# Optimization experiments

Hardware: AMD Instinct MI355X
Metric: run time of the kernel (lower is better)

## Reference

```python
import jax, jax.numpy as jnp
import numpy as np

SCALES = (3, 9, 17, 33)  # must be odd so padding=s//2 preserves spatial size


def _box_conv(img, s):
    # img: [B,1,H,W]; conv with an all-ones s x s kernel, 'same' padding for odd s
    k = jnp.ones((1, 1, s, s), img.dtype)
    p = s // 2
    return jax.lax.conv_general_dilated(
        img, k, window_strides=(1, 1), padding=[(p, p), (p, p)],
        dimension_numbers=("NCHW", "OIHW", "NCHW"))


def setup_inputs() -> dict:
    key = jax.random.key(0)
    B, C, H, W = 8, 3, 1024, 1024
    x = jax.random.normal(key, (B, C, H, W), dtype=jnp.float32)
    # mimicking sparse path-traced samples
    keep = jax.random.uniform(jax.random.fold_in(key, 1), (B, 1, H, W)) >= 0.3
    x = jnp.where(keep, x, 0.0)
    return {"x": x}


def reference(x):
    # F.conv2d(x, ones(1,3,1,1)/3) == per-pixel mean over the 3 channels
    lum = jnp.mean(x, axis=1, keepdims=True)          # [B,1,H,W]
    nonzero = (lum != 0).astype(lum.dtype)            # [B,1,H,W]
    feats = []
    for s in SCALES:
        count = _box_conv(nonzero, s)                 # number of nonzero pixels in window
        pool = _box_conv(lum, s) / jnp.maximum(count, 1.0)  # mean over nonzero pixels
        feats.append(count / float(s * s))            # percentage of nonzero pixels
        feats.append(pool)
    return jnp.concatenate(feats, axis=1)             # [B, 2*len(SCALES), H, W]
```

## Files before the change

kernel.cpp:

```cpp
#include <hip/hip_runtime.h>


constexpr int THREADS = 256;
constexpr int LOADW   = 256;
constexpr int HALO    = 17;
constexpr int COUT    = 223;
constexpr int RING2   = 19;
constexpr int ROWSEG  = 32;

constexpr int    Wc  = 1024;
constexpr int    Hc  = 1024;
constexpr size_t HWc = (size_t)Hc * Wc;

__device__ __forceinline__ void barrier_lds() {
    asm volatile("s_waitcnt lgkmcnt(0)" ::: "memory");
    __builtin_amdgcn_s_barrier();
    __builtin_amdgcn_sched_barrier(0);
}

template<int CTRL, int RM>
__device__ __forceinline__ int dppadd_i(int v) {
    int sh = __builtin_amdgcn_update_dpp(0, v, CTRL, RM, 0xF, true);
    return v + sh;
}

__device__ __forceinline__ int wave_iscan_i(int v) {
    v = dppadd_i<0x111, 0xF>(v);
    v = dppadd_i<0x112, 0xF>(v);
    v = dppadd_i<0x114, 0xF>(v);
    v = dppadd_i<0x118, 0xF>(v);
    v = dppadd_i<0x142, 0xA>(v);
    v = dppadd_i<0x143, 0xC>(v);
    return v;
}

__device__ __forceinline__ int sx16(unsigned v) {
    return (int)(short)(unsigned short)v;
}

__global__ __launch_bounds__(THREADS, 5)
void nzfeat_kernel(const float* __restrict__ x, float* __restrict__ out) {
    constexpr int   PP[4]   = {1, 4, 8, 16};
    constexpr float INVA[4] = {1.f/9.f, 1.f/81.f, 1.f/289.f, 1.f/1089.f};
    constexpr float INVQ    = 1.f / 1024.f;

    __shared__ unsigned int   ringL[RING2][LOADW];
    __shared__ unsigned short ringN[RING2][LOADW];
    __shared__ int2           wsum[2][2][4];

    const int t    = threadIdx.x;
    const int lane = t & 63;
    const int wv   = t >> 6;

    const int x0 = blockIdx.x * COUT;
    const int y0 = blockIdx.y * ROWSEG;
    const int b  = blockIdx.z;

    const int    gx   = x0 - HALO + t;
    const bool   gxok = (gx >= 0) && (gx < Wc);
    const int    gxc  = min(max(gx, 0), Wc - 1);
    const float* xb   = x + (size_t)b * 3 * HWc + gxc;

    auto load_row = [&](int r, float& a0, float& a1, float& a2) {
        const int rc = min(max(r, 0), Hc - 1);
        const float* p = xb + ((size_t)rc << 10);
        a0 = p[0]; a1 = p[HWc]; a2 = p[2 * HWc];
    };

    auto ps2  = [&](int j) { return (int)((unsigned)(j + 190) % (unsigned)RING2); };
    auto wpos = [&](int v) { return v >= RING2 ? v - RING2 : v; };
    auto wneg = [&](int v) { return v < 0 ? v + RING2 : v; };

    auto scan_local = [&](float c0, float c1, float c2, int r, int par, int which) -> int2 {
        float lum = 0.f;
        if (gxok && (unsigned)r < (unsigned)Hc)
            lum = (c0 + c1 + c2) * (1.0f / 3.0f);
        const bool nzb = (lum != 0.f);
        unsigned long long m = __ballot(nzb);
        int below = __builtin_amdgcn_mbcnt_hi((unsigned)(m >> 32),
                      __builtin_amdgcn_mbcnt_lo((unsigned)m, 0));
        int np = below + (nzb ? 1 : 0);
        int q  = (int)rintf(lum * 1024.f);
        int lp = wave_iscan_i(q);
        if (lane == 63) wsum[par][which][wv] = make_int2(lp, np);
        return make_int2(lp, np);
    };

    auto combine_write = [&](int par, int2 A, int2 Bv, int pslot) {
        int oAl = 0, oAn = 0, oBl = 0, oBn = 0;
        #pragma unroll
        for (int w2 = 0; w2 < 3; ++w2)
            if (w2 < wv) {
                int2 u = wsum[par][0][w2]; int2 v = wsum[par][1][w2];
                oAl += u.x; oAn += u.y; oBl += v.x; oBn += v.y;
            }
        unsigned llo = (unsigned)(A.x + oAl) & 0xFFFFu;
        unsigned lhi = (unsigned)(Bv.x + oBl) & 0xFFFFu;
        ringL[pslot][t] = (lhi << 16) | llo;
        unsigned nlo = (unsigned)(A.y + oAn) & 0xFFu;
        unsigned nhi = (unsigned)(Bv.y + oBn) & 0xFFu;
        ringN[pslot][t] = (unsigned short)((nhi << 8) | nlo);
    };

    auto rdAligned = [&](int s, int x1, int d, int& dl0, int& dl1,
                         int& dn0, int& dn1) {
        const unsigned int* Lp = &ringL[s][x1];
        unsigned w0 = Lp[0], w1 = Lp[d];
        dl0 = sx16(w1 - w0);
        dl1 = sx16((w1 >> 16) - (w0 >> 16));
        const unsigned short* Np = &ringN[s][x1];
        unsigned n0 = Np[0], n1 = Np[d];
        dn0 = (int)((n1 - n0) & 0xFFu);
        dn1 = (int)(((n1 >> 8) - (n0 >> 8)) & 0xFFu);
    };
    auto rdStraddle = [&](int sH, int sL2, int x1, int d, int& dA, int& dB,
                          int& nA, int& nB) {
        const unsigned int* LpH = &ringL[sH][x1];
        unsigned h0 = LpH[0], h1 = LpH[d];
        dA = sx16((h1 >> 16) - (h0 >> 16));
        const unsigned int* LpL = &ringL[sL2][x1];
        unsigned l0 = LpL[0], l1 = LpL[d];
        dB = sx16(l1 - l0);
        const unsigned short* NpH = &ringN[sH][x1];
        unsigned m0 = NpH[0], m1 = NpH[d];
        nA = (int)(((m1 >> 8) - (m0 >> 8)) & 0xFFu);
        const unsigned short* NpL = &ringN[sL2][x1];
        unsigned k0 = NpL[0], k1 = NpL[d];
        nB = (int)((k1 - k0) & 0xFFu);
    };

    float a0, a1, a2, b0c, b1c, b2c;
    load_row(y0 - 18, a0, a1, a2);
    load_row(y0 - 17, b0c, b1c, b2c);
    for (int i = 0; i < 17; ++i) {
        const int rA = y0 - 18 + 2 * i;
        float n0, n1, n2, m0, m1, m2;
        load_row(rA + 2, n0, n1, n2);
        load_row(rA + 3, m0, m1, m2);
        int2 A  = scan_local(a0, a1, a2, rA, i & 1, 0);
        int2 Bv = scan_local(b0c, b1c, b2c, rA + 1, i & 1, 1);
        barrier_lds();
        combine_write(i & 1, A, Bv, ps2(rA >> 1));
        a0 = n0; a1 = n1; a2 = n2; b0c = m0; b1c = m1; b2c = m2;
    }
    barrier_lds();

    const bool activeCol = (t < COUT) && (x0 + t < Wc);
    const int  tx = min(t, COUT - 1);
    float* outb = out + (size_t)b * 8 * HWc + (x0 + t);

    int vl[4], vn[4];
    #pragma unroll
    for (int i = 0; i < 4; ++i) {
        const int p  = PP[i];
        const int d  = 2 * p + 1;
        const int x1 = tx + HALO - p - 1;
        int sl = 0, sn = 0;
        for (int rr = y0 - 1 - p; rr <= y0 - 1 + p; ++rr) {
            const int s = ps2(rr >> 1);
            const unsigned int* Lp = &ringL[s][x1];
            unsigned w0 = Lp[0], w1 = Lp[d];
            const unsigned short* Np = &ringN[s][x1];
            unsigned n0 = Np[0], n1 = Np[d];
            if (rr & 1) {
                sl += sx16((w1 >> 16) - (w0 >> 16));
                sn += (int)(((n1 >> 8) - (n0 >> 8)) & 0xFFu);
            } else {
                sl += sx16(w1 - w0);
                sn += (int)((n1 - n0) & 0xFFu);
            }
        }
        vl[i] = sl; vn[i] = sn;
    }

    int pc = ps2(y0 >> 1);
    int pw = ps2((y0 >> 1) + 8);
    for (int k = 0; k <= ROWSEG / 2; ++k) {
        const bool doScan = (k < ROWSEG / 2);
        int2 A = make_int2(0, 0), Bv = make_int2(0, 0);
        float n0 = 0.f, n1 = 0.f, n2 = 0.f, m0 = 0.f, m1 = 0.f, m2 = 0.f;
        if (doScan) {
            const int wA = y0 + 2 * k + 16;
            if (k < ROWSEG / 2 - 1) {
                load_row(wA + 2, n0, n1, n2);
                load_row(wA + 3, m0, m1, m2);
            }
            A  = scan_local(a0, a1, a2, wA, k & 1, 0);
            Bv = scan_local(b0c, b1c, b2c, wA + 1, k & 1, 1);
        }
        barrier_lds();
        if (doScan) {
            combine_write(k & 1, A, Bv, pw);
            pw = wpos(pw + 1);
        }
        if (k >= 1) {
            const int ye = y0 + 2 * (k - 1);

            int eL0[4], eL1[4], eN0[4], eN1[4];
            int lL0[4], lL1[4], lN0[4], lN1[4];
            {
                const int d = 3, x1 = tx + HALO - 2;
                rdStraddle(pc, wpos(pc + 1), x1, d, eL0[0], eL1[0], eN0[0], eN1[0]);
                rdAligned (wneg(pc - 1),     x1, d, lL0[0], lL1[0], lN0[0], lN1[0]);
            }
            #pragma unroll
            for (int i = 1; i < 4; ++i) {
                const int p  = PP[i];
                const int d  = 2 * p + 1;
                const int x1 = tx + HALO - p - 1;
                rdAligned (wpos(pc + p / 2), x1, d, eL0[i], eL1[i], eN0[i], eN1[i]);
                rdStraddle(wneg(pc - p / 2 - 1), wneg(pc - p / 2), x1, d,
                           lL0[i], lL1[i], lN0[i], lN1[i]);
            }

            #pragma unroll
            for (int i = 0; i < 4; ++i) {
                vl[i] += eL0[i] - lL0[i];
                vn[i] += eN0[i] - lN0[i];
            }
            if (activeCol) {
                float* o = outb + ((size_t)ye << 10);
                #pragma unroll
                for (int i = 0; i < 4; ++i) {
                    float cnt = (float)vn[i];
                    o[(size_t)(2 * i) * HWc]     = cnt * INVA[i];
                    o[(size_t)(2 * i + 1) * HWc] =
                        (float)vl[i] * INVQ * __builtin_amdgcn_rcpf(fmaxf(cnt, 1.f));
                }
            }

            #pragma unroll
            for (int i = 0; i < 4; ++i) {
                vl[i] += eL1[i] - lL1[i];
                vn[i] += eN1[i] - lN1[i];
            }
            if (activeCol) {
                float* o = outb + ((size_t)(ye + 1) << 10);
                #pragma unroll
                for (int i = 0; i < 4; ++i) {
                    float cnt = (float)vn[i];
                    o[(size_t)(2 * i) * HWc]     = cnt * INVA[i];
                    o[(size_t)(2 * i + 1) * HWc] =
                        (float)vl[i] * INVQ * __builtin_amdgcn_rcpf(fmaxf(cnt, 1.f));
                }
            }

            pc = wpos(pc + 1);
        }
        a0 = n0; a1 = n1; a2 = n2; b0c = m0; b1c = m1; b2c = m2;
    }
}

extern "C" void kernel_launch(void* const* d_in, const int* in_sizes, int n_in,
                              void* d_out, int out_size, void* d_ws, size_t ws_size,
                              hipStream_t stream) {
    const float* x   = (const float*)d_in[0];
    float*       out = (float*)d_out;

    const int B = in_sizes[0] / (3 * Hc * Wc);

    dim3 grid((Wc + COUT - 1) / COUT, (Hc + ROWSEG - 1) / ROWSEG, B);
    nzfeat_kernel<<<grid, dim3(THREADS), 0, stream>>>(x, out);
}
```

Measured before the change: 110.7 us.

## Software-pipeline the ring scan, write and emit stages across loop iterations

Restructures the main row loop into a three-stage software pipeline. The LDS reads for the emit stage are issued right after the barrier and before the combine_write of the previous scan result, and the current row's scan runs while those reads are in flight. Scan results are carried in registers to the next iteration, which gives one more loop iteration of latency. The goal is to hide LDS read latency and shorten the critical path per barrier, at the cost of more live registers and changed ring slot timing.

```diff
diff --git a/kernel.cpp b/kernel.cpp
--- a/kernel.cpp
+++ b/kernel.cpp
@@ -100,33 +100,6 @@
         unsigned nlo = (unsigned)(A.y + oAn) & 0xFFu;
         unsigned nhi = (unsigned)(Bv.y + oBn) & 0xFFu;
         ringN[pslot][t] = (unsigned short)((nhi << 8) | nlo);
-    };
-
-    auto rdAligned = [&](int s, int x1, int d, int& dl0, int& dl1,
-                         int& dn0, int& dn1) {
-        const unsigned int* Lp = &ringL[s][x1];
-        unsigned w0 = Lp[0], w1 = Lp[d];
-        dl0 = sx16(w1 - w0);
-        dl1 = sx16((w1 >> 16) - (w0 >> 16));
-        const unsigned short* Np = &ringN[s][x1];
-        unsigned n0 = Np[0], n1 = Np[d];
-        dn0 = (int)((n1 - n0) & 0xFFu);
-        dn1 = (int)(((n1 >> 8) - (n0 >> 8)) & 0xFFu);
-    };
-    auto rdStraddle = [&](int sH, int sL2, int x1, int d, int& dA, int& dB,
-                          int& nA, int& nB) {
-        const unsigned int* LpH = &ringL[sH][x1];
-        unsigned h0 = LpH[0], h1 = LpH[d];
-        dA = sx16((h1 >> 16) - (h0 >> 16));
-        const unsigned int* LpL = &ringL[sL2][x1];
-        unsigned l0 = LpL[0], l1 = LpL[d];
-        dB = sx16(l1 - l0);
-        const unsigned short* NpH = &ringN[sH][x1];
-        unsigned m0 = NpH[0], m1 = NpH[d];
-        nA = (int)(((m1 >> 8) - (m0 >> 8)) & 0xFFu);
-        const unsigned short* NpL = &ringN[sL2][x1];
-        unsigned k0 = NpL[0], k1 = NpL[d];
-        nB = (int)((k1 - k0) & 0xFFu);
     };
 
     float a0, a1, a2, b0c, b1c, b2c;
@@ -173,44 +146,106 @@
         vl[i] = sl; vn[i] = sn;
     }
 
-    int pc = ps2(y0 >> 1);
-    int pw = ps2((y0 >> 1) + 8);
-    for (int k = 0; k <= ROWSEG / 2; ++k) {
-        const bool doScan = (k < ROWSEG / 2);
-        int2 A = make_int2(0, 0), Bv = make_int2(0, 0);
+    const int py0 = y0 >> 1;
+    int pc = ps2(py0);
+    int pw = ps2(py0 + 8);
+    int2 Acar = make_int2(0, 0), Bcar = make_int2(0, 0);
+
+    unsigned alW0[4], alW1[4], alN0[4], alN1[4];
+    unsigned stH0[4], stH1[4], stL0[4], stL1[4];
+    unsigned stM0[4], stM1[4], stQ0[4], stQ1[4];
+
+    for (int k = 0; k <= 17; ++k) {
+        const bool doLoad  = (k <= 14);
+        const bool doScan  = (k <= 15);
+        const bool doWrite = (k >= 1) && (k <= 16);
+        const bool doEmit  = (k >= 2);
+
         float n0 = 0.f, n1 = 0.f, n2 = 0.f, m0 = 0.f, m1 = 0.f, m2 = 0.f;
-        if (doScan) {
-            const int wA = y0 + 2 * k + 16;
-            if (k < ROWSEG / 2 - 1) {
-                load_row(wA + 2, n0, n1, n2);
-                load_row(wA + 3, m0, m1, m2);
-            }
-            A  = scan_local(a0, a1, a2, wA, k & 1, 0);
-            Bv = scan_local(b0c, b1c, b2c, wA + 1, k & 1, 1);
-        }
+        if (doLoad) {
+            load_row(y0 + 18 + 2 * k, n0, n1, n2);
+            load_row(y0 + 19 + 2 * k, m0, m1, m2);
+        }
+
         barrier_lds();
-        if (doScan) {
-            combine_write(k & 1, A, Bv, pw);
-            pw = wpos(pw + 1);
-        }
-        if (k >= 1) {
-            const int ye = y0 + 2 * (k - 1);
-
-            int eL0[4], eL1[4], eN0[4], eN1[4];
-            int lL0[4], lL1[4], lN0[4], lN1[4];
+
+        if (doEmit) {
             {
                 const int d = 3, x1 = tx + HALO - 2;
-                rdStraddle(pc, wpos(pc + 1), x1, d, eL0[0], eL1[0], eN0[0], eN1[0]);
-                rdAligned (wneg(pc - 1),     x1, d, lL0[0], lL1[0], lN0[0], lN1[0]);
+                const unsigned int*   LH = &ringL[pc][x1];
+                const unsigned int*   LL = &ringL[wpos(pc + 1)][x1];
+                const unsigned short* NH = &ringN[pc][x1];
+                const unsigned short* NL = &ringN[wpos(pc + 1)][x1];
+                stH0[0] = LH[0]; stH1[0] = LH[d];
+                stL0[0] = LL[0]; stL1[0] = LL[d];
+                stM0[0] = NH[0]; stM1[0] = NH[d];
+                stQ0[0] = NL[0]; stQ1[0] = NL[d];
+                const int sA = wneg(pc - 1);
+                const unsigned int*   LA = &ringL[sA][x1];
+                const unsigned short* NA = &ringN[sA][x1];
+                alW0[0] = LA[0]; alW1[0] = LA[d];
+                alN0[0] = NA[0]; alN1[0] = NA[d];
             }
             #pragma unroll
             for (int i = 1; i < 4; ++i) {
                 const int p  = PP[i];
                 const int d  = 2 * p + 1;
                 const int x1 = tx + HALO - p - 1;
-                rdAligned (wpos(pc + p / 2), x1, d, eL0[i], eL1[i], eN0[i], eN1[i]);
-                rdStraddle(wneg(pc - p / 2 - 1), wneg(pc - p / 2), x1, d,
-                           lL0[i], lL1[i], lN0[i], lN1[i]);
+                const int sA = wpos(pc + p / 2);
+                const unsigned int*   LA = &ringL[sA][x1];
+                const unsigned short* NA = &ringN[sA][x1];
+                alW0[i] = LA[0]; alW1[i] = LA[d];
+                alN0[i] = NA[0]; alN1[i] = NA[d];
+                const int sH = wneg(pc - p / 2 - 1);
+                const int sL = wneg(pc - p / 2);
+                const unsigned int*   LH = &ringL[sH][x1];
+                const unsigned int*   LL = &ringL[sL][x1];
+                const unsigned short* NH = &ringN[sH][x1];
+                const unsigned short* NL = &ringN[sL][x1];
+                stH0[i] = LH[0]; stH1[i] = LH[d];
+                stL0[i] = LL[0]; stL1[i] = LL[d];
+                stM0[i] = NH[0]; stM1[i] = NH[d];
+                stQ0[i] = NL[0]; stQ1[i] = NL[d];
+            }
+        }
+
+        if (doWrite) {
+            combine_write((k - 1) & 1, Acar, Bcar, pw);
+            pw = wpos(pw + 1);
+        }
+
+        int2 Anew = make_int2(0, 0), Bnew = make_int2(0, 0);
+        if (doScan) {
+            const int wA = y0 + 16 + 2 * k;
+            Anew = scan_local(a0, a1, a2, wA, k & 1, 0);
+            Bnew = scan_local(b0c, b1c, b2c, wA + 1, k & 1, 1);
+        }
+
+        if (doEmit) {
+            const int ye = y0 + 2 * (k - 2);
+
+            int eL0[4], eL1[4], eN0[4], eN1[4];
+            int lL0[4], lL1[4], lN0[4], lN1[4];
+            {
+                eL0[0] = sx16((stH1[0] >> 16) - (stH0[0] >> 16));
+                eL1[0] = sx16(stL1[0] - stL0[0]);
+                eN0[0] = (int)(((stM1[0] >> 8) - (stM0[0] >> 8)) & 0xFFu);
+                eN1[0] = (int)((stQ1[0] - stQ0[0]) & 0xFFu);
+                lL0[0] = sx16(alW1[0] - alW0[0]);
+                lL1[0] = sx16((alW1[0] >> 16) - (alW0[0] >> 16));
+                lN0[0] = (int)((alN1[0] - alN0[0]) & 0xFFu);
+                lN1[0] = (int)(((alN1[0] >> 8) - (alN0[0] >> 8)) & 0xFFu);
+            }
+            #pragma unroll
+            for (int i = 1; i < 4; ++i) {
+                eL0[i] = sx16(alW1[i] - alW0[i]);
+                eL1[i] = sx16((alW1[i] >> 16) - (alW0[i] >> 16));
+                eN0[i] = (int)((alN1[i] - alN0[i]) & 0xFFu);
+                eN1[i] = (int)(((alN1[i] >> 8) - (alN0[i] >> 8)) & 0xFFu);
+                lL0[i] = sx16((stH1[i] >> 16) - (stH0[i] >> 16));
+                lL1[i] = sx16(stL1[i] - stL0[i]);
+                lN0[i] = (int)(((stM1[i] >> 8) - (stM0[i] >> 8)) & 0xFFu);
+                lN1[i] = (int)((stQ1[i] - stQ0[i]) & 0xFFu);
             }
 
             #pragma unroll
@@ -247,6 +282,8 @@
 
             pc = wpos(pc + 1);
         }
+
+        Acar = Anew; Bcar = Bnew;
         a0 = n0; a1 = n1; a2 = n2; b0c = m0; b1c = m1; b2c = m2;
     }
 }
```

Measured after the change: 111.7 us. About the same (+0.9%).
